# Optimization experiments

Measured on AMD Instinct MI355X. Metric: run time of the kernel, lower is better.

## Reference

```python
import jax, jax.numpy as jnp
import numpy as np

BN_EPS = 1e-5
K = 3  # number of nearest neighbors for interpolation


def setup_inputs() -> dict:
    key = jax.random.key(0)
    ks = jax.random.split(key, 16)
    B, N1, N2 = 8, 8192, 2048
    C2, C1, H = 256, 128, 256  # in_channels, skip_channels, out_channels
    total_in = C2 + C1
    inp = {
        "xyz1": jax.random.normal(ks[0], (B, 3, N1), dtype=jnp.float32),
        "xyz2": jax.random.normal(ks[1], (B, 3, N2), dtype=jnp.float32),
        "features1": jax.random.normal(ks[2], (B, C1, N1), dtype=jnp.float32),
        "features2": jax.random.normal(ks[3], (B, C2, N2), dtype=jnp.float32),
        # SharedMLP([total_in, H, H]): two 1x1 Conv1d + BatchNorm1d (eval mode) + ReLU
        "w1": jax.random.normal(ks[4], (H, total_in), dtype=jnp.float32) * 0.05,
        "b1": jax.random.normal(ks[5], (H,), dtype=jnp.float32) * 0.01,
        "g1": 1.0 + 0.1 * jax.random.normal(ks[6], (H,), dtype=jnp.float32),
        "be1": 0.1 * jax.random.normal(ks[7], (H,), dtype=jnp.float32),
        "m1": 0.1 * jax.random.normal(ks[8], (H,), dtype=jnp.float32),
        "v1": 0.5 + jax.random.uniform(ks[9], (H,), dtype=jnp.float32),
        "w2": jax.random.normal(ks[10], (H, H), dtype=jnp.float32) * 0.05,
        "b2": jax.random.normal(ks[11], (H,), dtype=jnp.float32) * 0.01,
        "g2": 1.0 + 0.1 * jax.random.normal(ks[12], (H,), dtype=jnp.float32),
        "be2": 0.1 * jax.random.normal(ks[13], (H,), dtype=jnp.float32),
        "m2": 0.1 * jax.random.normal(ks[14], (H,), dtype=jnp.float32),
        "v2": 0.5 + jax.random.uniform(ks[15], (H,), dtype=jnp.float32),
    }
    return inp


def _conv_bn_relu(x, w, b, g, be, m, v):
    # x: [B, Cin, N], w: [Cout, Cin] (1x1 conv), BN in eval mode
    y = jnp.einsum("oc,bcn->bon", w, x) + b[None, :, None]
    y = (y - m[None, :, None]) * (g / jnp.sqrt(v + BN_EPS))[None, :, None] + be[None, :, None]
    return jax.nn.relu(y)


def reference(xyz1, xyz2, features1, features2,
              w1, b1, g1, be1, m1, v1,
              w2, b2, g2, be2, m2, v2):
    # --- squared pairwise distances [B, N1, N2] ---
    x1 = jnp.transpose(xyz1, (0, 2, 1))  # [B, N1, 3]
    x2 = jnp.transpose(xyz2, (0, 2, 1))  # [B, N2, 3]
    sq = (jnp.sum(x1 * x1, axis=-1, keepdims=True)
          + jnp.sum(x2 * x2, axis=-1)[:, None, :]
          - 2.0 * jnp.einsum("bnd,bmd->bnm", x1, x2))
    # --- k=3 nearest neighbors (smallest sq distances) ---
    neg_d, idx = jax.lax.top_k(-sq, K)          # [B, N1, K]
    dist = jnp.maximum(-neg_d, 1e-10)
    weight = 1.0 / dist
    weight = weight / jnp.sum(weight, axis=-1, keepdims=True)  # [B, N1, K]
    # --- gather neighbor features and inverse-distance interpolate ---
    feat2_t = jnp.transpose(features2, (0, 2, 1))              # [B, N2, C2]
    neighbor = jax.vmap(lambda f, i: f[i])(feat2_t, idx)       # [B, N1, K, C2]
    interp = jnp.einsum("bnkc,bnk->bnc", neighbor, weight)     # [B, N1, C2]
    interp = jnp.transpose(interp, (0, 2, 1))                  # [B, C2, N1]
    # --- concat skip features and shared MLP ---
    x = jnp.concatenate([interp, features1], axis=1)           # [B, C2+C1, N1]
    x = _conv_bn_relu(x, w1, b1, g1, be1, m1, v1)
    x = _conv_bn_relu(x, w2, b2, g2, be2, m2, v2)
    return x
```

## Files before the change

kernel.cpp:

```cpp
#include <hip/hip_runtime.h>
#include <hip/hip_bf16.h>

typedef unsigned short u16;
typedef __attribute__((ext_vector_type(4))) float f32x4;
typedef __attribute__((ext_vector_type(8))) short short8;

#define BN_EPS 1e-5f

__device__ __forceinline__ u16 f2b(float x) {
  union { float f; unsigned int u; } v; v.f = x;
  unsigned int r = (v.u + 0x7FFFu + ((v.u >> 16) & 1u)) >> 16;
  return (u16)r;
}
__device__ __forceinline__ float b2f(u16 u) {
  union { unsigned int u; float f; } v; v.u = ((unsigned int)u) << 16;
  return v.f;
}
__device__ __forceinline__ float asf(unsigned u) {
  union { unsigned u; float f; } v; v.u = u; return v.f;
}

__global__ void prep_transpose_kernel(
    const float* __restrict__ f2, u16* __restrict__ f2t,
    const float* __restrict__ w1, const float* __restrict__ b1,
    const float* __restrict__ g1, const float* __restrict__ be1,
    const float* __restrict__ m1, const float* __restrict__ v1,
    const float* __restrict__ w2, const float* __restrict__ b2,
    const float* __restrict__ g2, const float* __restrict__ be2,
    const float* __restrict__ m2, const float* __restrict__ v2,
    u16* __restrict__ w1b, u16* __restrict__ w2b,
    float* __restrict__ al1, float* __restrict__ bt1,
    float* __restrict__ al2, float* __restrict__ bt2) {
  __shared__ float tile[32][33];
  int t = threadIdx.x;
  int blk = blockIdx.x;
  if (blk < 4096) {
    int tx = t & 31, ty = t >> 5;
    int b = (blk >> 9) & 7;
    int n2t = (blk & 63) * 32, ct = ((blk >> 6) & 7) * 32;
#pragma unroll
    for (int i = 0; i < 4; ++i) {
      int c = ct + ty + i * 8;
      tile[ty + i * 8][tx] = f2[((size_t)b * 256 + c) * 2048 + n2t + tx];
    }
    __syncthreads();
#pragma unroll
    for (int i = 0; i < 4; ++i) {
      int n2 = n2t + ty + i * 8;
      f2t[((size_t)b * 2048 + n2) * 256 + ct + tx] = f2b(tile[tx][ty + i * 8]);
    }
  } else if (blk < 4480) {
    int id = (blk - 4096) * 256 + t;
    unsigned o = (unsigned)id / 384u;
    unsigned c = (unsigned)id % 384u;
    w1b[(c >> 5) * 8192 + o * 32 + (c & 31)] = f2b(w1[id]);
  } else if (blk < 4736) {
    int j = (blk - 4480) * 256 + t;
    unsigned o = (unsigned)j >> 8;
    unsigned c = (unsigned)j & 255u;
    w2b[(c >> 5) * 8192 + o * 32 + (c & 31)] = f2b(w2[j]);
  } else if (blk == 4736) {
    float a = g1[t] / sqrtf(v1[t] + BN_EPS);
    al1[t] = a;
    bt1[t] = (b1[t] - m1[t]) * a + be1[t];
  } else {
    float a = g2[t] / sqrtf(v2[t] + BN_EPS);
    al2[t] = a;
    bt2[t] = (b2[t] - m2[t]) * a + be2[t];
  }
}

__global__ __launch_bounds__(256) void knn_interp_kernel(
    const float* __restrict__ xyz1, const float* __restrict__ xyz2,
    const float* __restrict__ f1, const u16* __restrict__ f2t,
    u16* __restrict__ xb) {
  union Lds {
    struct { float4 pts[2048]; float md[256 * 3]; int mi[256 * 3]; } a;
    float f1t[128 * 65];
  };
  __shared__ Lds lds;
  __shared__ float wts[64 * 3];
  __shared__ int idxs[64 * 3];

  int t = threadIdx.x;
  int b = blockIdx.x >> 7;
  int n1_0 = (blockIdx.x & 127) * 64;
  int panel = blockIdx.x;

  const float* x2 = xyz2 + b * 3 * 2048;
  for (int j = t; j < 2048; j += 256) {
    float cx = x2[j], cy = x2[2048 + j], cz = x2[4096 + j];
    float nsq = (cx * cx + cy * cy) + cz * cz;
    lds.a.pts[j] = make_float4(cx, cy, cz, nsq);
  }
  __syncthreads();

  const float* x1 = xyz1 + b * 3 * 8192;

  {
    int p = t & 63, s = t >> 6;
    int n1 = n1_0 + p;
    float bx = x1[n1], by = x1[8192 + n1], bz = x1[16384 + n1];
    float nx = -2.f * bx, ny = -2.f * by, nz = -2.f * bz;
    float d0 = 3.4e38f, d1 = 3.4e38f, d2 = 3.4e38f;
    int i0 = 0, i1 = 0, i2 = 0;
    int jb = s * 512;
#pragma unroll 4
    for (int jj = 0; jj < 512; ++jj) {
      float4 c = lds.a.pts[jb + jj];
      float sq = fmaf(nx, c.x, fmaf(ny, c.y, fmaf(nz, c.z, c.w)));
      int j = jb + jj;
      bool c0 = sq < d0, c1 = sq < d1, c2 = sq < d2;
      i2 = c1 ? i1 : (c2 ? j : i2);
      i1 = c0 ? i0 : (c1 ? j : i1);
      i0 = c0 ? j : i0;
      d2 = __builtin_amdgcn_fmed3f(sq, d1, d2);
      d1 = __builtin_amdgcn_fmed3f(sq, d0, d1);
      d0 = fminf(sq, d0);
    }
    lds.a.md[t * 3 + 0] = d0; lds.a.md[t * 3 + 1] = d1; lds.a.md[t * 3 + 2] = d2;
    lds.a.mi[t * 3 + 0] = i0; lds.a.mi[t * 3 + 1] = i1; lds.a.mi[t * 3 + 2] = i2;
  }
  __syncthreads();
  if (t < 64) {
    float d0 = 3.4e38f, d1 = 3.4e38f, d2 = 3.4e38f;
    int i0 = 0, i1 = 0, i2 = 0;
#pragma unroll
    for (int s = 0; s < 4; ++s) {
#pragma unroll
      for (int k = 0; k < 3; ++k) {
        float d = lds.a.md[(s * 64 + t) * 3 + k];
        int i = lds.a.mi[(s * 64 + t) * 3 + k];
        bool c0 = d < d0, c1 = d < d1, c2 = d < d2;
        i2 = c1 ? i1 : (c2 ? i : i2);
        i1 = c0 ? i0 : (c1 ? i : i1);
        i0 = c0 ? i : i0;
        d2 = c1 ? d1 : (c2 ? d : d2);
        d1 = c0 ? d0 : (c1 ? d : d1);
        d0 = c0 ? d : d0;
      }
    }
    int n1 = n1_0 + t;
    float bx = x1[n1], by = x1[8192 + n1], bz = x1[16384 + n1];
    float nn = (bx * bx + by * by) + bz * bz;
    float e0 = fmaxf(d0 + nn, 1e-10f), e1 = fmaxf(d1 + nn, 1e-10f), e2 = fmaxf(d2 + nn, 1e-10f);
    float w0 = 1.0f / e0, w1 = 1.0f / e1, w2 = 1.0f / e2;
    float sm = (w0 + w1) + w2;
    wts[t * 3 + 0] = w0 / sm; wts[t * 3 + 1] = w1 / sm; wts[t * 3 + 2] = w2 / sm;
    idxs[t * 3 + 0] = i0 * 256; idxs[t * 3 + 1] = i1 * 256; idxs[t * 3 + 2] = i2 * 256;
  }
  __syncthreads();

  {
    const u16* f2tb = f2t + (size_t)b * 2048 * 256;
    int tc = t & 127;
    int ph = t >> 7;
    int ce = (2 * tc) & 31;
    size_t xbase = (size_t)panel * 24576 + (size_t)(tc >> 4) * 2048 + ce;
#pragma unroll 4
    for (int p2 = 0; p2 < 32; ++p2) {
      int p = p2 * 2 + ph;
      int j0 = idxs[p * 3 + 0], j1 = idxs[p * 3 + 1], j2 = idxs[p * 3 + 2];
      float w0 = wts[p * 3 + 0], w1 = wts[p * 3 + 1], w2 = wts[p * 3 + 2];
      unsigned a0 = *(const unsigned*)&f2tb[j0 + 2 * tc];
      unsigned a1 = *(const unsigned*)&f2tb[j1 + 2 * tc];
      unsigned a2 = *(const unsigned*)&f2tb[j2 + 2 * tc];
      float vlo = (w0 * asf(a0 << 16) + w1 * asf(a1 << 16)) + w2 * asf(a2 << 16);
      float vhi = (w0 * asf(a0 & 0xffff0000u) + w1 * asf(a1 & 0xffff0000u))
                  + w2 * asf(a2 & 0xffff0000u);
      unsigned pk = (unsigned)f2b(vlo) | ((unsigned)f2b(vhi) << 16);
      *(unsigned*)&xb[xbase + (size_t)p * 32] = pk;
    }
  }
  __syncthreads();

  {
    const float* f1b = f1 + (size_t)b * 128 * 8192 + n1_0;
    for (int it = 0; it < 32; ++it) {
      int c = it * 4 + (t >> 6);
      int n = t & 63;
      lds.f1t[c * 65 + n] = f1b[(size_t)c * 8192 + n];
    }
    __syncthreads();
    for (int it = 0; it < 32; ++it) {
      int v = it * 256 + t;
      int c = v & 127, p = v >> 7;
      float val = lds.f1t[c * 65 + p];
      xb[(size_t)panel * 24576 + (size_t)(8 + (c >> 5)) * 2048 + p * 32 + (c & 31)] = f2b(val);
    }
  }
}

__global__ __launch_bounds__(256) void gemm_fused_kernel(
    const u16* __restrict__ xin, const u16* __restrict__ w1b,
    const u16* __restrict__ w2b,
    const float* __restrict__ al1, const float* __restrict__ bt1,
    const float* __restrict__ al2, const float* __restrict__ bt2,
    float* __restrict__ fout) {
  __shared__ u16 y1t[8 * 64 * 40];
  int t = threadIdx.x;
  int panel = blockIdx.x;
  int w = t >> 6, lane = t & 63, l15 = lane & 15, quad = lane >> 4;

  f32x4 acc[4][4];
#pragma unroll
  for (int m = 0; m < 4; ++m)
#pragma unroll
    for (int n = 0; n < 4; ++n)
      acc[m][n] = (f32x4){0.f, 0.f, 0.f, 0.f};

  {
    const u16* aw = w1b + (size_t)(w * 64 + l15) * 32 + quad * 8;
    const u16* bx = xin + (size_t)panel * (12 * 2048) + (size_t)l15 * 32 + quad * 8;
    short8 af[2][4], bf[2][4];
#pragma unroll
    for (int m = 0; m < 4; ++m)
      af[0][m] = *(const short8*)(aw + m * 512);
#pragma unroll
    for (int n = 0; n < 4; ++n)
      bf[0][n] = *(const short8*)(bx + n * 512);
#pragma unroll
    for (int kt = 0; kt < 12; ++kt) {
      int cur = kt & 1, nxt = cur ^ 1;
      if (kt < 11) {
#pragma unroll
        for (int m = 0; m < 4; ++m)
          af[nxt][m] = *(const short8*)(aw + (kt + 1) * 8192 + m * 512);
#pragma unroll
        for (int n = 0; n < 4; ++n)
          bf[nxt][n] = *(const short8*)(bx + (kt + 1) * 2048 + n * 512);
      }
#pragma unroll
      for (int m = 0; m < 4; ++m)
#pragma unroll
        for (int n = 0; n < 4; ++n)
          acc[m][n] = __builtin_amdgcn_mfma_f32_16x16x32_bf16(af[cur][m], bf[cur][n], acc[m][n], 0, 0, 0);
    }
  }

  {
    float al[4][4], bt[4][4];
#pragma unroll
    for (int m = 0; m < 4; ++m)
#pragma unroll
      for (int r = 0; r < 4; ++r) {
        int o = w * 64 + m * 16 + quad * 4 + r;
        al[m][r] = al1[o];
        bt[m][r] = bt1[o];
      }
#pragma unroll
    for (int m = 0; m < 4; ++m) {
      int kt2 = w * 2 + (m >> 1);
      int osub = (m & 1) * 16 + quad * 4;
#pragma unroll
      for (int n = 0; n < 4; ++n) {
        int col = n * 16 + l15;
        ushort4 pk;
        pk.x = f2b(fmaxf(fmaf(al[m][0], acc[m][n][0], bt[m][0]), 0.f));
        pk.y = f2b(fmaxf(fmaf(al[m][1], acc[m][n][1], bt[m][1]), 0.f));
        pk.z = f2b(fmaxf(fmaf(al[m][2], acc[m][n][2], bt[m][2]), 0.f));
        pk.w = f2b(fmaxf(fmaf(al[m][3], acc[m][n][3], bt[m][3]), 0.f));
        *(ushort4*)&y1t[(kt2 * 64 + col) * 40 + osub] = pk;
      }
    }
  }
  __syncthreads();

#pragma unroll
  for (int m = 0; m < 4; ++m)
#pragma unroll
    for (int n = 0; n < 4; ++n)
      acc[m][n] = (f32x4){0.f, 0.f, 0.f, 0.f};
  {
    const u16* aw = w2b + (size_t)(w * 64 + l15) * 32 + quad * 8;
    short8 af[2][4];
#pragma unroll
    for (int m = 0; m < 4; ++m)
      af[0][m] = *(const short8*)(aw + m * 512);
#pragma unroll
    for (int kt = 0; kt < 8; ++kt) {
      int cur = kt & 1, nxt = cur ^ 1;
      if (kt < 7) {
#pragma unroll
        for (int m = 0; m < 4; ++m)
          af[nxt][m] = *(const short8*)(aw + (kt + 1) * 8192 + m * 512);
      }
      short8 bf[4];
#pragma unroll
      for (int n = 0; n < 4; ++n)
        bf[n] = *(const short8*)&y1t[(kt * 64 + n * 16 + l15) * 40 + quad * 8];
#pragma unroll
      for (int m = 0; m < 4; ++m)
#pragma unroll
        for (int n = 0; n < 4; ++n)
          acc[m][n] = __builtin_amdgcn_mfma_f32_16x16x32_bf16(af[cur][m], bf[n], acc[m][n], 0, 0, 0);
    }
  }

  {
    float al[4][4], bt[4][4];
#pragma unroll
    for (int m = 0; m < 4; ++m)
#pragma unroll
      for (int r = 0; r < 4; ++r) {
        int o = w * 64 + m * 16 + quad * 4 + r;
        al[m][r] = al2[o];
        bt[m][r] = bt2[o];
      }
    int bb = panel >> 7;
    int n1base = (panel & 127) * 64;
#pragma unroll
    for (int m = 0; m < 4; ++m)
#pragma unroll
      for (int n = 0; n < 4; ++n) {
        int col = n * 16 + l15;
#pragma unroll
        for (int r = 0; r < 4; ++r) {
          int o = w * 64 + m * 16 + quad * 4 + r;
          float vv = fmaxf(fmaf(al[m][r], acc[m][n][r], bt[m][r]), 0.f);
          fout[(size_t)(bb * 256 + o) * 8192 + n1base + col] = vv;
        }
      }
  }
}

extern "C" void kernel_launch(void* const* d_in, const int* in_sizes, int n_in,
                              void* d_out, int out_size, void* d_ws, size_t ws_size,
                              hipStream_t stream) {
  const float* xyz1 = (const float*)d_in[0];
  const float* xyz2 = (const float*)d_in[1];
  const float* f1   = (const float*)d_in[2];
  const float* f2   = (const float*)d_in[3];
  const float* w1   = (const float*)d_in[4];
  const float* b1   = (const float*)d_in[5];
  const float* g1   = (const float*)d_in[6];
  const float* be1  = (const float*)d_in[7];
  const float* m1   = (const float*)d_in[8];
  const float* v1   = (const float*)d_in[9];
  const float* w2   = (const float*)d_in[10];
  const float* b2   = (const float*)d_in[11];
  const float* g2   = (const float*)d_in[12];
  const float* be2  = (const float*)d_in[13];
  const float* m2   = (const float*)d_in[14];
  const float* v2   = (const float*)d_in[15];

  char* ws = (char*)d_ws;
  u16* xb   = (u16*)(ws);
  u16* f2t  = (u16*)(ws + 50331648);
  u16* w1b  = (u16*)(ws + 83886080);
  u16* w2b  = (u16*)(ws + 84082688);
  float* al1 = (float*)(ws + 84213760);
  float* bt1 = (float*)(ws + 84214784);
  float* al2 = (float*)(ws + 84215808);
  float* bt2 = (float*)(ws + 84216832);
  float* out = (float*)d_out;

  prep_transpose_kernel<<<4738, 256, 0, stream>>>(
      f2, f2t, w1, b1, g1, be1, m1, v1, w2, b2, g2, be2, m2, v2,
      w1b, w2b, al1, bt1, al2, bt2);
  knn_interp_kernel<<<1024, 256, 0, stream>>>(xyz1, xyz2, f1, f2t, xb);
  gemm_fused_kernel<<<1024, 256, 0, stream>>>(xb, w1b, w2b, al1, bt1, al2, bt2, out);
}
```

Before: 225.3 us.

## Read skip features directly in GEMM instead of staging through bf16 buffer

The skip-connection features (features1) are no longer transposed and converted to bf16 by the knn kernel and written into the intermediate panel buffer. The fused GEMM now loads fp32 features1 straight from global memory for the last four K-tiles and converts them to bf16 in registers before the MFMA. This removes a write and a re-read of the skip-channel panel and shrinks the panel stride. It also stores the partial neighbor indices as u16 in LDS, which lowers LDS use. The cost is strided scalar fp32 loads inside the GEMM loop, which may be less coalesced and add register pressure.

```diff
diff --git a/kernel.cpp b/kernel.cpp
--- a/kernel.cpp
+++ b/kernel.cpp
@@ -72,13 +72,10 @@
 
 __global__ __launch_bounds__(256) void knn_interp_kernel(
     const float* __restrict__ xyz1, const float* __restrict__ xyz2,
-    const float* __restrict__ f1, const u16* __restrict__ f2t,
-    u16* __restrict__ xb) {
-  union Lds {
-    struct { float4 pts[2048]; float md[256 * 3]; int mi[256 * 3]; } a;
-    float f1t[128 * 65];
-  };
-  __shared__ Lds lds;
+    const u16* __restrict__ f2t, u16* __restrict__ xb) {
+  __shared__ float4 pts[2048];
+  __shared__ float md[256 * 3];
+  __shared__ u16 mi[256 * 3];
   __shared__ float wts[64 * 3];
   __shared__ int idxs[64 * 3];
 
@@ -91,7 +88,7 @@
   for (int j = t; j < 2048; j += 256) {
     float cx = x2[j], cy = x2[2048 + j], cz = x2[4096 + j];
     float nsq = (cx * cx + cy * cy) + cz * cz;
-    lds.a.pts[j] = make_float4(cx, cy, cz, nsq);
+    pts[j] = make_float4(cx, cy, cz, nsq);
   }
   __syncthreads();
 
@@ -107,7 +104,7 @@
     int jb = s * 512;
 #pragma unroll 4
     for (int jj = 0; jj < 512; ++jj) {
-      float4 c = lds.a.pts[jb + jj];
+      float4 c = pts[jb + jj];
       float sq = fmaf(nx, c.x, fmaf(ny, c.y, fmaf(nz, c.z, c.w)));
       int j = jb + jj;
       bool c0 = sq < d0, c1 = sq < d1, c2 = sq < d2;
@@ -118,8 +115,8 @@
       d1 = __builtin_amdgcn_fmed3f(sq, d0, d1);
       d0 = fminf(sq, d0);
     }
-    lds.a.md[t * 3 + 0] = d0; lds.a.md[t * 3 + 1] = d1; lds.a.md[t * 3 + 2] = d2;
-    lds.a.mi[t * 3 + 0] = i0; lds.a.mi[t * 3 + 1] = i1; lds.a.mi[t * 3 + 2] = i2;
+    md[t * 3 + 0] = d0; md[t * 3 + 1] = d1; md[t * 3 + 2] = d2;
+    mi[t * 3 + 0] = (u16)i0; mi[t * 3 + 1] = (u16)i1; mi[t * 3 + 2] = (u16)i2;
   }
   __syncthreads();
   if (t < 64) {
@@ -129,8 +126,8 @@
     for (int s = 0; s < 4; ++s) {
 #pragma unroll
       for (int k = 0; k < 3; ++k) {
-        float d = lds.a.md[(s * 64 + t) * 3 + k];
-        int i = lds.a.mi[(s * 64 + t) * 3 + k];
+        float d = md[(s * 64 + t) * 3 + k];
+        int i = (int)mi[(s * 64 + t) * 3 + k];
         bool c0 = d < d0, c1 = d < d1, c2 = d < d2;
         i2 = c1 ? i1 : (c2 ? i : i2);
         i1 = c0 ? i0 : (c1 ? i : i1);
@@ -156,7 +153,7 @@
     int tc = t & 127;
     int ph = t >> 7;
     int ce = (2 * tc) & 31;
-    size_t xbase = (size_t)panel * 24576 + (size_t)(tc >> 4) * 2048 + ce;
+    size_t xbase = (size_t)panel * 16384 + (size_t)(tc >> 4) * 2048 + ce;
 #pragma unroll 4
     for (int p2 = 0; p2 < 32; ++p2) {
       int p = p2 * 2 + ph;
@@ -172,28 +169,11 @@
       *(unsigned*)&xb[xbase + (size_t)p * 32] = pk;
     }
   }
-  __syncthreads();
-
-  {
-    const float* f1b = f1 + (size_t)b * 128 * 8192 + n1_0;
-    for (int it = 0; it < 32; ++it) {
-      int c = it * 4 + (t >> 6);
-      int n = t & 63;
-      lds.f1t[c * 65 + n] = f1b[(size_t)c * 8192 + n];
-    }
-    __syncthreads();
-    for (int it = 0; it < 32; ++it) {
-      int v = it * 256 + t;
-      int c = v & 127, p = v >> 7;
-      float val = lds.f1t[c * 65 + p];
-      xb[(size_t)panel * 24576 + (size_t)(8 + (c >> 5)) * 2048 + p * 32 + (c & 31)] = f2b(val);
-    }
-  }
 }
 
 __global__ __launch_bounds__(256) void gemm_fused_kernel(
-    const u16* __restrict__ xin, const u16* __restrict__ w1b,
-    const u16* __restrict__ w2b,
+    const u16* __restrict__ xin, const float* __restrict__ f1,
+    const u16* __restrict__ w1b, const u16* __restrict__ w2b,
     const float* __restrict__ al1, const float* __restrict__ bt1,
     const float* __restrict__ al2, const float* __restrict__ bt2,
     float* __restrict__ fout) {
@@ -201,6 +181,8 @@
   int t = threadIdx.x;
   int panel = blockIdx.x;
   int w = t >> 6, lane = t & 63, l15 = lane & 15, quad = lane >> 4;
+  int bb = panel >> 7;
+  int n1base = (panel & 127) * 64;
 
   f32x4 acc[4][4];
 #pragma unroll
@@ -211,14 +193,16 @@
 
   {
     const u16* aw = w1b + (size_t)(w * 64 + l15) * 32 + quad * 8;
-    const u16* bx = xin + (size_t)panel * (12 * 2048) + (size_t)l15 * 32 + quad * 8;
-    short8 af[2][4], bf[2][4];
+    const u16* bx = xin + (size_t)panel * 16384 + (size_t)l15 * 32 + quad * 8;
+    const float* f1lane = f1 + ((size_t)bb * 128 + quad * 8) * 8192 + n1base + l15;
+    short8 af[2][4], bfx[2][4];
+    float fr[4][8];
 #pragma unroll
     for (int m = 0; m < 4; ++m)
       af[0][m] = *(const short8*)(aw + m * 512);
 #pragma unroll
     for (int n = 0; n < 4; ++n)
-      bf[0][n] = *(const short8*)(bx + n * 512);
+      bfx[0][n] = *(const short8*)(bx + n * 512);
 #pragma unroll
     for (int kt = 0; kt < 12; ++kt) {
       int cur = kt & 1, nxt = cur ^ 1;
@@ -226,15 +210,46 @@
 #pragma unroll
         for (int m = 0; m < 4; ++m)
           af[nxt][m] = *(const short8*)(aw + (kt + 1) * 8192 + m * 512);
-#pragma unroll
-        for (int n = 0; n < 4; ++n)
-          bf[nxt][n] = *(const short8*)(bx + (kt + 1) * 2048 + n * 512);
+      }
+      if (kt < 7) {
+#pragma unroll
+        for (int n = 0; n < 4; ++n)
+          bfx[nxt][n] = *(const short8*)(bx + (kt + 1) * 2048 + n * 512);
+      }
+      if (kt == 7) {
+#pragma unroll
+        for (int n = 0; n < 4; ++n)
+#pragma unroll
+          for (int r = 0; r < 8; ++r)
+            fr[n][r] = f1lane[(size_t)r * 8192 + n * 16];
+      }
+      short8 bfu[4];
+      if (kt < 8) {
+#pragma unroll
+        for (int n = 0; n < 4; ++n)
+          bfu[n] = bfx[cur][n];
+      } else {
+#pragma unroll
+        for (int n = 0; n < 4; ++n) {
+          union { ushort us[8]; short8 s; } cv;
+#pragma unroll
+          for (int r = 0; r < 8; ++r)
+            cv.us[r] = f2b(fr[n][r]);
+          bfu[n] = cv.s;
+        }
+        if (kt < 11) {
+#pragma unroll
+          for (int n = 0; n < 4; ++n)
+#pragma unroll
+            for (int r = 0; r < 8; ++r)
+              fr[n][r] = f1lane[(size_t)((kt - 7) * 32 + r) * 8192 + n * 16];
+        }
       }
 #pragma unroll
       for (int m = 0; m < 4; ++m)
 #pragma unroll
         for (int n = 0; n < 4; ++n)
-          acc[m][n] = __builtin_amdgcn_mfma_f32_16x16x32_bf16(af[cur][m], bf[cur][n], acc[m][n], 0, 0, 0);
+          acc[m][n] = __builtin_amdgcn_mfma_f32_16x16x32_bf16(af[cur][m], bfu[n], acc[m][n], 0, 0, 0);
     }
   }
 
@@ -307,8 +322,6 @@
         al[m][r] = al2[o];
         bt[m][r] = bt2[o];
       }
-    int bb = panel >> 7;
-    int n1base = (panel & 127) * 64;
 #pragma unroll
     for (int m = 0; m < 4; ++m)
 #pragma unroll
@@ -358,6 +371,6 @@
   prep_transpose_kernel<<<4738, 256, 0, stream>>>(
       f2, f2t, w1, b1, g1, be1, m1, v1, w2, b2, g2, be2, m2, v2,
       w1b, w2b, al1, bt1, al2, bt2);
-  knn_interp_kernel<<<1024, 256, 0, stream>>>(xyz1, xyz2, f1, f2t, xb);
-  gemm_fused_kernel<<<1024, 256, 0, stream>>>(xb, w1b, w2b, al1, bt1, al2, bt2, out);
-}
+  knn_interp_kernel<<<1024, 256, 0, stream>>>(xyz1, xyz2, f2t, xb);
+  gemm_fused_kernel<<<1024, 256, 0, stream>>>(xb, f1, w1b, w2b, al1, bt1, al2, bt2, out);
+}
```

Measured after the change: 229.9 us. 2.1% more time.

## Move skip-feature transpose and point prep into prep kernel; read candidates from global

Applied to the files above, without the earlier changes.

The features1 transpose into the bf16 GEMM input buffer moves from the KNN kernel into extra blocks of the prep kernel, and the xyz2 norm precompute is written to a global SoA buffer. The KNN kernel no longer stages the 2048 candidate points in LDS. Instead its inner loop reads the x/y/z/norm arrays directly through uniform global (likely scalar/cache) loads, with the unroll raised to 8. This cuts LDS use and a barrier phase to raise occupancy, at the risk of slower global-memory latency in the hottest loop.

```diff
diff --git a/kernel.cpp b/kernel.cpp
--- a/kernel.cpp
+++ b/kernel.cpp
@@ -20,7 +20,7 @@
   union { unsigned u; float f; } v; v.u = u; return v.f;
 }
 
-__global__ void prep_transpose_kernel(
+__global__ void prep_kernel(
     const float* __restrict__ f2, u16* __restrict__ f2t,
     const float* __restrict__ w1, const float* __restrict__ b1,
     const float* __restrict__ g1, const float* __restrict__ be1,
@@ -28,10 +28,13 @@
     const float* __restrict__ w2, const float* __restrict__ b2,
     const float* __restrict__ g2, const float* __restrict__ be2,
     const float* __restrict__ m2, const float* __restrict__ v2,
+    const float* __restrict__ xyz2, const float* __restrict__ f1,
     u16* __restrict__ w1b, u16* __restrict__ w2b,
     float* __restrict__ al1, float* __restrict__ bt1,
-    float* __restrict__ al2, float* __restrict__ bt2) {
+    float* __restrict__ al2, float* __restrict__ bt2,
+    float* __restrict__ c4, u16* __restrict__ xb) {
   __shared__ float tile[32][33];
+  __shared__ float tile2[32 * 65];
   int t = threadIdx.x;
   int blk = blockIdx.x;
   if (blk < 4096) {
@@ -63,22 +66,49 @@
     float a = g1[t] / sqrtf(v1[t] + BN_EPS);
     al1[t] = a;
     bt1[t] = (b1[t] - m1[t]) * a + be1[t];
-  } else {
+  } else if (blk == 4737) {
     float a = g2[t] / sqrtf(v2[t] + BN_EPS);
     al2[t] = a;
     bt2[t] = (b2[t] - m2[t]) * a + be2[t];
+  } else if (blk < 4802) {
+    int idx = (blk - 4738) * 256 + t;
+    int b = idx >> 11, j = idx & 2047;
+    float cx = xyz2[b * 6144 + j];
+    float cy = xyz2[b * 6144 + 2048 + j];
+    float cz = xyz2[b * 6144 + 4096 + j];
+    float nsq = (cx * cx + cy * cy) + cz * cz;
+    c4[b * 8192 + j] = cx;
+    c4[b * 8192 + 2048 + j] = cy;
+    c4[b * 8192 + 4096 + j] = cz;
+    c4[b * 8192 + 6144 + j] = nsq;
+  } else {
+    int idx = blk - 4802;
+    int b = idx >> 9;
+    int rest = idx & 511;
+    int ct = (rest >> 7) * 32;
+    int nt = (rest & 127) * 64;
+#pragma unroll
+    for (int i = 0; i < 8; ++i) {
+      int c = (t >> 6) + i * 4;
+      int n = t & 63;
+      tile2[c * 65 + n] = f1[((size_t)(b * 128 + ct + c)) * 8192 + nt + n];
+    }
+    __syncthreads();
+    size_t base = (size_t)(b * 128 + (nt >> 6)) * 24576 + (size_t)(8 + (ct >> 5)) * 2048;
+#pragma unroll
+    for (int i = 0; i < 8; ++i) {
+      int p = (t >> 5) + i * 8;
+      int c = t & 31;
+      xb[base + p * 32 + c] = f2b(tile2[c * 65 + p]);
+    }
   }
 }
 
 __global__ __launch_bounds__(256) void knn_interp_kernel(
-    const float* __restrict__ xyz1, const float* __restrict__ xyz2,
-    const float* __restrict__ f1, const u16* __restrict__ f2t,
-    u16* __restrict__ xb) {
-  union Lds {
-    struct { float4 pts[2048]; float md[256 * 3]; int mi[256 * 3]; } a;
-    float f1t[128 * 65];
-  };
-  __shared__ Lds lds;
+    const float* __restrict__ xyz1, const float* __restrict__ c4,
+    const u16* __restrict__ f2t, u16* __restrict__ xb) {
+  __shared__ float md[256 * 3];
+  __shared__ int mi[256 * 3];
   __shared__ float wts[64 * 3];
   __shared__ int idxs[64 * 3];
 
@@ -87,14 +117,6 @@
   int n1_0 = (blockIdx.x & 127) * 64;
   int panel = blockIdx.x;
 
-  const float* x2 = xyz2 + b * 3 * 2048;
-  for (int j = t; j < 2048; j += 256) {
-    float cx = x2[j], cy = x2[2048 + j], cz = x2[4096 + j];
-    float nsq = (cx * cx + cy * cy) + cz * cz;
-    lds.a.pts[j] = make_float4(cx, cy, cz, nsq);
-  }
-  __syncthreads();
-
   const float* x1 = xyz1 + b * 3 * 8192;
 
   {
@@ -102,14 +124,17 @@
     int n1 = n1_0 + p;
     float bx = x1[n1], by = x1[8192 + n1], bz = x1[16384 + n1];
     float nx = -2.f * bx, ny = -2.f * by, nz = -2.f * bz;
+    const float* cxp = c4 + b * 8192;
+    const float* cyp = cxp + 2048;
+    const float* czp = cxp + 4096;
+    const float* cwp = cxp + 6144;
     float d0 = 3.4e38f, d1 = 3.4e38f, d2 = 3.4e38f;
     int i0 = 0, i1 = 0, i2 = 0;
     int jb = s * 512;
-#pragma unroll 4
+#pragma unroll 8
     for (int jj = 0; jj < 512; ++jj) {
-      float4 c = lds.a.pts[jb + jj];
-      float sq = fmaf(nx, c.x, fmaf(ny, c.y, fmaf(nz, c.z, c.w)));
       int j = jb + jj;
+      float sq = fmaf(nx, cxp[j], fmaf(ny, cyp[j], fmaf(nz, czp[j], cwp[j])));
       bool c0 = sq < d0, c1 = sq < d1, c2 = sq < d2;
       i2 = c1 ? i1 : (c2 ? j : i2);
       i1 = c0 ? i0 : (c1 ? j : i1);
@@ -118,8 +143,8 @@
       d1 = __builtin_amdgcn_fmed3f(sq, d0, d1);
       d0 = fminf(sq, d0);
     }
-    lds.a.md[t * 3 + 0] = d0; lds.a.md[t * 3 + 1] = d1; lds.a.md[t * 3 + 2] = d2;
-    lds.a.mi[t * 3 + 0] = i0; lds.a.mi[t * 3 + 1] = i1; lds.a.mi[t * 3 + 2] = i2;
+    md[t * 3 + 0] = d0; md[t * 3 + 1] = d1; md[t * 3 + 2] = d2;
+    mi[t * 3 + 0] = i0; mi[t * 3 + 1] = i1; mi[t * 3 + 2] = i2;
   }
   __syncthreads();
   if (t < 64) {
@@ -129,8 +154,8 @@
     for (int s = 0; s < 4; ++s) {
 #pragma unroll
       for (int k = 0; k < 3; ++k) {
-        float d = lds.a.md[(s * 64 + t) * 3 + k];
-        int i = lds.a.mi[(s * 64 + t) * 3 + k];
+        float d = md[(s * 64 + t) * 3 + k];
+        int i = mi[(s * 64 + t) * 3 + k];
         bool c0 = d < d0, c1 = d < d1, c2 = d < d2;
         i2 = c1 ? i1 : (c2 ? i : i2);
         i1 = c0 ? i0 : (c1 ? i : i1);
@@ -172,23 +197,6 @@
       *(unsigned*)&xb[xbase + (size_t)p * 32] = pk;
     }
   }
-  __syncthreads();
-
-  {
-    const float* f1b = f1 + (size_t)b * 128 * 8192 + n1_0;
-    for (int it = 0; it < 32; ++it) {
-      int c = it * 4 + (t >> 6);
-      int n = t & 63;
-      lds.f1t[c * 65 + n] = f1b[(size_t)c * 8192 + n];
-    }
-    __syncthreads();
-    for (int it = 0; it < 32; ++it) {
-      int v = it * 256 + t;
-      int c = v & 127, p = v >> 7;
-      float val = lds.f1t[c * 65 + p];
-      xb[(size_t)panel * 24576 + (size_t)(8 + (c >> 5)) * 2048 + p * 32 + (c & 31)] = f2b(val);
-    }
-  }
 }
 
 __global__ __launch_bounds__(256) void gemm_fused_kernel(
@@ -211,7 +219,7 @@
 
   {
     const u16* aw = w1b + (size_t)(w * 64 + l15) * 32 + quad * 8;
-    const u16* bx = xin + (size_t)panel * (12 * 2048) + (size_t)l15 * 32 + quad * 8;
+    const u16* bx = xin + (size_t)panel * 24576 + (size_t)l15 * 32 + quad * 8;
     short8 af[2][4], bf[2][4];
 #pragma unroll
     for (int m = 0; m < 4; ++m)
@@ -347,6 +355,7 @@
   char* ws = (char*)d_ws;
   u16* xb   = (u16*)(ws);
   u16* f2t  = (u16*)(ws + 50331648);
+  float* c4 = (float*)(ws + 58720256);
   u16* w1b  = (u16*)(ws + 83886080);
   u16* w2b  = (u16*)(ws + 84082688);
   float* al1 = (float*)(ws + 84213760);
@@ -355,9 +364,9 @@
   float* bt2 = (float*)(ws + 84216832);
   float* out = (float*)d_out;
 
-  prep_transpose_kernel<<<4738, 256, 0, stream>>>(
+  prep_kernel<<<8898, 256, 0, stream>>>(
       f2, f2t, w1, b1, g1, be1, m1, v1, w2, b2, g2, be2, m2, v2,
-      w1b, w2b, al1, bt1, al2, bt2);
-  knn_interp_kernel<<<1024, 256, 0, stream>>>(xyz1, xyz2, f1, f2t, xb);
+      xyz2, f1, w1b, w2b, al1, bt1, al2, bt2, c4, xb);
+  knn_interp_kernel<<<1024, 256, 0, stream>>>(xyz1, c4, f2t, xb);
   gemm_fused_kernel<<<1024, 256, 0, stream>>>(xb, w1b, w2b, al1, bt1, al2, bt2, out);
 }
```

Result: slower. 243.8 us (+8.2%).
